# Kernel optimization log

Hardware: AMD Instinct MI355X
Metric: run time of the kernel (lower is better)

Reference implementation:

```python
import jax, jax.numpy as jnp
import numpy as np
import math

D = 768
H = 12
DK = D // H
DI = 3072
EPS_LN = 1e-12
NEG = -1e9


def layernorm(x, g, b):
    mu = jnp.mean(x, axis=-1, keepdims=True)
    var = jnp.mean(jnp.square(x - mu), axis=-1, keepdims=True)
    return (x - mu) * jax.lax.rsqrt(var + EPS_LN) * g + b


def setup_inputs() -> dict:
    key = jax.random.key(0)
    ks = jax.random.split(key, 16)
    B, S = 16, 512
    sd = 0.02
    inp = {
        "hidden_states": jax.random.normal(ks[0], (B, S, D), dtype=jnp.float32),
        "constituent_prior": jnp.zeros((B, S, S), dtype=jnp.float32),
        "attention_mask": jnp.ones((B, S), dtype=jnp.int32),
        # MultiHeadedAttention: 4 linears (q, k, v, out)
        "Wq": jax.random.normal(ks[1], (D, D)) * sd, "bq": jnp.zeros((D,)),
        "Wk": jax.random.normal(ks[2], (D, D)) * sd, "bk": jnp.zeros((D,)),
        "Wv": jax.random.normal(ks[3], (D, D)) * sd, "bv": jnp.zeros((D,)),
        "Wo": jax.random.normal(ks[4], (D, D)) * sd, "bo": jnp.zeros((D,)),
        # GroupAttention: key/query linears + LayerNorm
        "gWk": jax.random.normal(ks[5], (D, D)) * sd, "gbk": jnp.zeros((D,)),
        "gWq": jax.random.normal(ks[6], (D, D)) * sd, "gbq": jnp.zeros((D,)),
        "g_ln_g": jnp.ones((D,)), "g_ln_b": jnp.zeros((D,)),
        # BertIntermediate / BertOutput
        "Wi": jax.random.normal(ks[7], (D, DI)) * sd, "bi": jnp.zeros((DI,)),
        "Wout": jax.random.normal(ks[8], (DI, D)) * sd, "bout": jnp.zeros((D,)),
        "ln_g": jnp.ones((D,)), "ln_b": jnp.zeros((D,)),
    }
    return {k: v.astype(jnp.float32) if v.dtype == jnp.float32 or jnp.issubdtype(v.dtype, jnp.floating) else v for k, v in inp.items()}


def group_attention(x, attention_mask, prior, gWk, gbk, gWq, gbq, g_ln_g, g_ln_b):
    B, S, _ = x.shape
    a = jnp.eye(S, k=1, dtype=jnp.float32)      # super-diagonal
    c = jnp.eye(S, k=-1, dtype=jnp.float32)     # sub-diagonal
    eye = jnp.eye(S, dtype=jnp.float32)
    tri = jnp.triu(jnp.ones((S, S), dtype=jnp.float32))  # upper-tri incl. diag

    h = layernorm(x, g_ln_g, g_ln_b)
    k = h @ gWk + gbk
    q = h @ gWq + gbq
    scores = jnp.einsum("bsd,btd->bst", q, k) / D
    # mask[b,i,j] = attention_mask[b,j] & (a+c)[i,j]  (only +/-1 neighbors)
    mask = attention_mask.astype(jnp.float32)[:, None, :] * (a + c)[None]
    scores = jnp.where(mask == 0, NEG, scores)
    neigh = jax.nn.softmax(scores, axis=-1)
    neigh = jnp.sqrt(neigh * jnp.swapaxes(neigh, -2, -1) + 1e-9)
    neigh = prior + (1.0 - prior) * neigh

    # prefix log-sums along the super-diagonal via triangular matmuls
    t = jnp.where(a[None] == 0, 0.0, jnp.log(neigh + 1e-9)) @ tri
    C = jnp.exp(jnp.einsum("ij,bjk->bik", tri, t))
    C = jnp.where((tri - eye)[None] == 0, 0.0, C)   # keep strictly upper tri
    C = C + jnp.swapaxes(C, -2, -1) + jnp.where(eye[None] == 0, 1e-9, neigh)
    return C, neigh


def multi_head_attention(x, group_prob, attention_mask, Wq, bq, Wk, bk, Wv, bv, Wo, bo):
    B, S, _ = x.shape
    def split(y):  # [B,S,D] -> [B,H,S,DK]
        return y.reshape(B, S, H, DK).transpose(0, 2, 1, 3)
    q = split(x @ Wq + bq)
    k = split(x @ Wk + bk)
    v = split(x @ Wv + bv)
    scores = jnp.einsum("bhsd,bhtd->bhst", q, k) / math.sqrt(DK)
    eye = jnp.eye(S, dtype=jnp.int32)
    # combined mask: allow key j if attention_mask[b,j] or j == i (diagonal)
    cm = (attention_mask[:, None, None, :] | eye[None, None]) != 0
    scores = jnp.where(cm, scores, NEG)
    p = jax.nn.softmax(scores, axis=-1) * group_prob[:, None]  # [B,H,S,S]
    out = jnp.einsum("bhst,bhtd->bhsd", p, v)
    out = out.transpose(0, 2, 1, 3).reshape(B, S, D)
    return out @ Wo + bo


def reference(hidden_states, constituent_prior, attention_mask,
              Wq, bq, Wk, bk, Wv, bv, Wo, bo,
              gWk, gbk, gWq, gbq, g_ln_g, g_ln_b,
              Wi, bi, Wout, bout, ln_g, ln_b):
    C, neigh = group_attention(hidden_states, attention_mask, constituent_prior,
                               gWk, gbk, gWq, gbq, g_ln_g, g_ln_b)
    attn_out = multi_head_attention(hidden_states, C, attention_mask,
                                    Wq, bq, Wk, bk, Wv, bv, Wo, bo)
    inter = jax.nn.gelu(attn_out @ Wi + bi, approximate=False)
    layer_out = layernorm(inter @ Wout + bout + attn_out, ln_g, ln_b)
    return (layer_out, C, neigh, attn_out)
```

## Files before the change

kernel.cpp:

```cpp
#include <hip/hip_runtime.h>
#include <math.h>

typedef unsigned short ushort_t;
typedef __attribute__((ext_vector_type(8))) short bf16x8;
typedef __attribute__((ext_vector_type(4))) float f32x4;

#define Dt 768
#define Mrows 8192

__device__ __forceinline__ ushort_t f2b(float f) {
    union { float f; unsigned int u; } v; v.f = f;
    unsigned int u = v.u;
    unsigned int r = (u + 0x7fffu + ((u >> 16) & 1u)) >> 16;
    return (ushort_t)r;
}
__device__ __forceinline__ float b2f(ushort_t u) {
    union { unsigned int u; float f; } v; v.u = ((unsigned int)u) << 16;
    return v.f;
}
__device__ __forceinline__ f32x4 mfma16(bf16x8 a, bf16x8 b, f32x4 c) {
    return __builtin_amdgcn_mfma_f32_16x16x32_bf16(a, b, c, 0, 0, 0);
}
__device__ __forceinline__ float gelu_exact(float v) {
    return 0.5f * v * (1.0f + erff(v * 0.70710678118654752f));
}
__device__ __forceinline__ void gl2lds16(const ushort_t* g, ushort_t* l) {
    __builtin_amdgcn_global_load_lds((const __attribute__((address_space(1))) void*)g,
                                     (__attribute__((address_space(3))) void*)l,
                                     16, 0, 0);
}

__global__ __launch_bounds__(256)
void tconv_kernel(const float* __restrict__ in, ushort_t* __restrict__ out,
                  int K, int N)
{
    __shared__ float T[32][33];
    int t = threadIdx.x;
    int n0 = blockIdx.x * 32, k0 = blockIdx.y * 32;
    int r = t >> 3, c4 = (t & 7) * 4;
    float4 v = *(const float4*)(in + (size_t)(k0 + r) * N + n0 + c4);
    T[r][c4] = v.x; T[r][c4 + 1] = v.y; T[r][c4 + 2] = v.z; T[r][c4 + 3] = v.w;
    __syncthreads();
    int nl = t >> 3, k4 = (t & 7) * 4;
    unsigned int lo = (unsigned int)f2b(T[k4][nl]) | ((unsigned int)f2b(T[k4 + 1][nl]) << 16);
    unsigned int hi = (unsigned int)f2b(T[k4 + 2][nl]) | ((unsigned int)f2b(T[k4 + 3][nl]) << 16);
    uint2 o; o.x = lo; o.y = hi;
    *(uint2*)(out + (size_t)(n0 + nl) * K + k0 + k4) = o;
}

__global__ __launch_bounds__(256)
void xconv_kernel(const float* __restrict__ in, ushort_t* __restrict__ out, int n4)
{
    int gid = blockIdx.x * 256 + threadIdx.x;
    if (gid >= n4) return;
    float4 v = ((const float4*)in)[gid];
    unsigned int lo = (unsigned int)f2b(v.x) | ((unsigned int)f2b(v.y) << 16);
    unsigned int hi = (unsigned int)f2b(v.z) | ((unsigned int)f2b(v.w) << 16);
    uint2 o; o.x = lo; o.y = hi;
    *(uint2*)(out + (size_t)gid * 4) = o;
}

__global__ __launch_bounds__(256)
void bconcat_kernel(const float* bq, const float* bk, const float* bv,
                    const float* gbq, const float* gbk,
                    float* bqkv, float* gbqk)
{
    int g = blockIdx.x * 256 + threadIdx.x;
    if (g < 768)       bqkv[g] = bq[g];
    else if (g < 1536) bqkv[g] = bk[g - 768];
    else if (g < 2304) bqkv[g] = bv[g - 1536];
    else if (g < 3072) gbqk[g - 2304] = gbq[g - 2304];
    else if (g < 3840) gbqk[g - 2304] = gbk[g - 3072];
}

template<int BF16OUT>
__global__ __launch_bounds__(256)
void ln_kernel(const float* __restrict__ x, const float* __restrict__ g,
               const float* __restrict__ be, void* __restrict__ outv)
{
    int row = blockIdx.x;
    const float* xr = x + (size_t)row * Dt;
    int t = threadIdx.x;
    float v0 = xr[t], v1 = xr[t + 256], v2 = xr[t + 512];
    float s = v0 + v1 + v2;
    #pragma unroll
    for (int off = 32; off; off >>= 1) s += __shfl_xor(s, off, 64);
    __shared__ float r1[4], r2[4];
    if ((t & 63) == 0) r1[t >> 6] = s;
    __syncthreads();
    float mu = (r1[0] + r1[1] + r1[2] + r1[3]) * (1.0f / Dt);
    float d0 = v0 - mu, d1 = v1 - mu, d2 = v2 - mu;
    float sq = d0 * d0 + d1 * d1 + d2 * d2;
    #pragma unroll
    for (int off = 32; off; off >>= 1) sq += __shfl_xor(sq, off, 64);
    if ((t & 63) == 0) r2[t >> 6] = sq;
    __syncthreads();
    float var = (r2[0] + r2[1] + r2[2] + r2[3]) * (1.0f / Dt);
    float rs = 1.0f / sqrtf(var + 1e-12f);
    float o0 = d0 * rs * g[t]       + be[t];
    float o1 = d1 * rs * g[t + 256] + be[t + 256];
    float o2 = d2 * rs * g[t + 512] + be[t + 512];
    if (BF16OUT) {
        ushort_t* orow = (ushort_t*)outv + (size_t)row * Dt;
        orow[t] = f2b(o0); orow[t + 256] = f2b(o1); orow[t + 512] = f2b(o2);
    } else {
        float* orow = (float*)outv + (size_t)row * Dt;
        orow[t] = o0; orow[t + 256] = o1; orow[t + 512] = o2;
    }
}

enum { EPI_BF16 = 1, EPI_QKV = 2, EPI_DUAL = 3, EPI_GELU = 4, EPI_RES = 5, EPI_ACC = 6 };

template<int BN, int EPI>
__global__ __launch_bounds__(256)
void gemm128(const ushort_t* __restrict__ A, const ushort_t* __restrict__ Bt,
             const float* __restrict__ bias, const float* __restrict__ res,
             float* __restrict__ Cf, ushort_t* __restrict__ O0,
             ushort_t* __restrict__ O1, ushort_t* __restrict__ O2,
             int K, int ldb, int ldc)
{
    constexpr int NF = BN / 32;
    __shared__ ushort_t As[128 * 32];
    __shared__ ushort_t Bs[BN * 32];
    int t = threadIdx.x;
    int w = t >> 6, l = t & 63;
    int wr = w >> 1, wc = w & 1;
    int lr = l & 15, lg = l >> 4;
    int bn = blockIdx.x * BN;
    int bm = blockIdx.y * 128;

    const ushort_t* gA0 = A + (size_t)(bm + (t >> 2)) * K + ((t & 3) << 3);
    const ushort_t* gA1 = A + (size_t)(bm + 64 + (t >> 2)) * K + ((t & 3) << 3);
    const ushort_t* gB0 = Bt + (size_t)(bn + (t >> 2)) * ldb + ((t & 3) << 3);
    const ushort_t* gB1 = (BN == 128) ?
        Bt + (size_t)(bn + 64 + (t >> 2)) * ldb + ((t & 3) << 3) : nullptr;
    ushort_t* lA0 = As + (w << 9);
    ushort_t* lA1 = As + 2048 + (w << 9);
    ushort_t* lB0 = Bs + (w << 9);
    ushort_t* lB1 = Bs + 2048 + (w << 9);

    f32x4 acc[4][NF];
    #pragma unroll
    for (int m = 0; m < 4; ++m)
        #pragma unroll
        for (int n = 0; n < NF; ++n) acc[m][n] = (f32x4)0.0f;

    for (int k0 = 0; k0 < K; k0 += 32) {
        gl2lds16(gA0 + k0, lA0);
        gl2lds16(gA1 + k0, lA1);
        gl2lds16(gB0 + k0, lB0);
        if (BN == 128) gl2lds16(gB1 + k0, lB1);
        __syncthreads();
        bf16x8 af[4], bfv[NF];
        #pragma unroll
        for (int m = 0; m < 4; ++m)
            af[m] = *(const bf16x8*)&As[(wr * 64 + m * 16 + lr) * 32 + lg * 8];
        #pragma unroll
        for (int n = 0; n < NF; ++n)
            bfv[n] = *(const bf16x8*)&Bs[(wc * (BN / 2) + n * 16 + lr) * 32 + lg * 8];
        __builtin_amdgcn_s_setprio(1);
        #pragma unroll
        for (int m = 0; m < 4; ++m)
            #pragma unroll
            for (int n = 0; n < NF; ++n)
                acc[m][n] = mfma16(af[m], bfv[n], acc[m][n]);
        __builtin_amdgcn_s_setprio(0);
        __syncthreads();
    }

    #pragma unroll
    for (int m = 0; m < 4; ++m) {
        int row0 = bm + wr * 64 + m * 16 + lg * 4;
        #pragma unroll
        for (int n = 0; n < NF; ++n) {
            int ng = bn + wc * (BN / 2) + n * 16 + lr;
            float v0 = acc[m][n][0], v1 = acc[m][n][1];
            float v2 = acc[m][n][2], v3 = acc[m][n][3];
            if (EPI != EPI_ACC) {
                float bv = bias[ng];
                v0 += bv; v1 += bv; v2 += bv; v3 += bv;
            }
            if (EPI == EPI_BF16) {
                O0[(size_t)(row0 + 0) * ldc + ng] = f2b(v0);
                O0[(size_t)(row0 + 1) * ldc + ng] = f2b(v1);
                O0[(size_t)(row0 + 2) * ldc + ng] = f2b(v2);
                O0[(size_t)(row0 + 3) * ldc + ng] = f2b(v3);
            } else if (EPI == EPI_QKV) {
                if (bn < 768) {
                    O0[(size_t)(row0 + 0) * 768 + ng] = f2b(v0 * 0.125f);
                    O0[(size_t)(row0 + 1) * 768 + ng] = f2b(v1 * 0.125f);
                    O0[(size_t)(row0 + 2) * 768 + ng] = f2b(v2 * 0.125f);
                    O0[(size_t)(row0 + 3) * 768 + ng] = f2b(v3 * 0.125f);
                } else if (bn < 1536) {
                    int c = ng - 768;
                    O1[(size_t)(row0 + 0) * 768 + c] = f2b(v0);
                    O1[(size_t)(row0 + 1) * 768 + c] = f2b(v1);
                    O1[(size_t)(row0 + 2) * 768 + c] = f2b(v2);
                    O1[(size_t)(row0 + 3) * 768 + c] = f2b(v3);
                } else {
                    int dk = ng - 1536;
                    unsigned int lo = (unsigned int)f2b(v0) | ((unsigned int)f2b(v1) << 16);
                    unsigned int hi = (unsigned int)f2b(v2) | ((unsigned int)f2b(v3) << 16);
                    uint2 o; o.x = lo; o.y = hi;
                    *(uint2*)(O2 + (size_t)dk * Mrows + row0) = o;
                }
            } else if (EPI == EPI_DUAL) {
                Cf[(size_t)(row0 + 0) * ldc + ng] = v0;
                Cf[(size_t)(row0 + 1) * ldc + ng] = v1;
                Cf[(size_t)(row0 + 2) * ldc + ng] = v2;
                Cf[(size_t)(row0 + 3) * ldc + ng] = v3;
                O0[(size_t)(row0 + 0) * ldc + ng] = f2b(v0);
                O0[(size_t)(row0 + 1) * ldc + ng] = f2b(v1);
                O0[(size_t)(row0 + 2) * ldc + ng] = f2b(v2);
                O0[(size_t)(row0 + 3) * ldc + ng] = f2b(v3);
            } else if (EPI == EPI_GELU) {
                O0[(size_t)(row0 + 0) * ldc + ng] = f2b(gelu_exact(v0));
                O0[(size_t)(row0 + 1) * ldc + ng] = f2b(gelu_exact(v1));
                O0[(size_t)(row0 + 2) * ldc + ng] = f2b(gelu_exact(v2));
                O0[(size_t)(row0 + 3) * ldc + ng] = f2b(gelu_exact(v3));
            } else if (EPI == EPI_RES) {
                Cf[(size_t)(row0 + 0) * ldc + ng] = v0 + res[(size_t)(row0 + 0) * Dt + ng];
                Cf[(size_t)(row0 + 1) * ldc + ng] = v1 + res[(size_t)(row0 + 1) * Dt + ng];
                Cf[(size_t)(row0 + 2) * ldc + ng] = v2 + res[(size_t)(row0 + 2) * Dt + ng];
                Cf[(size_t)(row0 + 3) * ldc + ng] = v3 + res[(size_t)(row0 + 3) * Dt + ng];
            } else if (EPI == EPI_ACC) {
                Cf[(size_t)(row0 + 0) * ldc + ng] += v0;
                Cf[(size_t)(row0 + 1) * ldc + ng] += v1;
                Cf[(size_t)(row0 + 2) * ldc + ng] += v2;
                Cf[(size_t)(row0 + 3) * ldc + ng] += v3;
            }
        }
    }
}

__global__ __launch_bounds__(256)
void group_scores_kernel(const ushort_t* __restrict__ GQK, const int* __restrict__ am,
                         float* __restrict__ smU, float* __restrict__ smD,
                         int* __restrict__ emptyF)
{
    int gi = blockIdx.x;
    int b = gi >> 9, s = gi & 511;
    int t = threadIdx.x;
    const ushort_t* qr = GQK + (size_t)gi * 1536;
    bool hasU = (s < 511) && (am[(b << 9) + s + 1] != 0);
    bool hasD = (s > 0)   && (am[(b << 9) + s - 1] != 0);
    float su = 0.0f, sd = 0.0f;
    if (hasU) {
        const ushort_t* kr = GQK + (size_t)(gi + 1) * 1536 + 768;
        for (int c = t; c < Dt; c += 256) su += b2f(qr[c]) * b2f(kr[c]);
    }
    if (hasD) {
        const ushort_t* kr = GQK + (size_t)(gi - 1) * 1536 + 768;
        for (int c = t; c < Dt; c += 256) sd += b2f(qr[c]) * b2f(kr[c]);
    }
    #pragma unroll
    for (int off = 32; off; off >>= 1) { su += __shfl_xor(su, off, 64); sd += __shfl_xor(sd, off, 64); }
    __shared__ float rU[4], rD[4];
    if ((t & 63) == 0) { rU[t >> 6] = su; rD[t >> 6] = sd; }
    __syncthreads();
    if (t == 0) {
        su = (rU[0] + rU[1] + rU[2] + rU[3]) * (1.0f / Dt);
        sd = (rD[0] + rD[1] + rD[2] + rD[3]) * (1.0f / Dt);
        float u, d2; int emp = 0;
        if (hasU && hasD) {
            float m = fmaxf(su, sd);
            float eu = __expf(su - m), ed = __expf(sd - m);
            float inv = 1.0f / (eu + ed);
            u = eu * inv; d2 = ed * inv;
        } else if (hasU) { u = 1.0f; d2 = 0.0f; }
        else if (hasD)   { u = 0.0f; d2 = 1.0f; }
        else { u = d2 = 1.0f / 512.0f; emp = 1; }
        smU[gi] = u; smD[gi] = d2; emptyF[gi] = emp;
    }
}

__global__ __launch_bounds__(512)
void neigh_kernel(const float* __restrict__ prior,
                  const float* __restrict__ smU, const float* __restrict__ smD,
                  const int* __restrict__ emptyF, float* __restrict__ ne_out)
{
    int bi = blockIdx.x;
    int j  = threadIdx.x;
    int b = bi >> 9, i = bi & 511;
    int bj = (b << 9) + j;
    const float invS = 1.0f / 512.0f;
    float fij, fji;
    if (j == i + 1)      { fij = smU[bi]; fji = smD[bj]; }
    else if (j == i - 1) { fij = smD[bi]; fji = smU[bj]; }
    else { fij = emptyF[bi] ? invS : 0.0f; fji = emptyF[bj] ? invS : 0.0f; }
    float val = sqrtf(fij * fji + 1e-9f);
    float pr = prior[(size_t)bi * 512 + j];
    ne_out[(size_t)bi * 512 + j] = pr + (1.0f - pr) * val;
}

__global__ __launch_bounds__(64)
void prefix_kernel(const float* __restrict__ ne, float* __restrict__ P)
{
    int b = blockIdx.x;
    int l = threadIdx.x;
    float lv[8];
    float run = 0.0f;
    #pragma unroll
    for (int e = 0; e < 8; ++e) {
        int j = l * 8 + e;
        float lj = 0.0f;
        if (j < 511) lj = logf(ne[((size_t)(b * 512 + j)) * 512 + (j + 1)] + 1e-9f);
        lv[e] = run;
        run += lj;
    }
    float tot = run;
    float scan = tot;
    #pragma unroll
    for (int off = 1; off < 64; off <<= 1) {
        float n = __shfl_up(scan, off, 64);
        if (l >= off) scan += n;
    }
    float excl = scan - tot;
    #pragma unroll
    for (int e = 0; e < 8; ++e)
        P[b * 512 + l * 8 + e] = excl + lv[e];
}

__global__ __launch_bounds__(512)
void cfill_kernel(const float* __restrict__ P, const float* __restrict__ ne,
                  float* __restrict__ C_out)
{
    int bi = blockIdx.x;
    int j = threadIdx.x;
    int b = bi >> 9, i = bi & 511;
    float pi = P[bi], pj = P[(b << 9) + j];
    float v;
    if (j > i)      v = expf(pj - pi) + 1e-9f;
    else if (j < i) v = expf(pi - pj) + 1e-9f;
    else            v = ne[(size_t)bi * 512 + i];
    C_out[(size_t)bi * 512 + j] = v;
}

__global__ __launch_bounds__(256)
void mha_mfma(const ushort_t* __restrict__ q, const ushort_t* __restrict__ k,
              const ushort_t* __restrict__ vt, const int* __restrict__ am,
              const float* __restrict__ Cmat, ushort_t* __restrict__ ctx)
{
    __shared__ ushort_t Qs[64][72];
    __shared__ ushort_t Ks[64][72];
    __shared__ ushort_t Vs[64][72];
    __shared__ ushort_t Ps[64][72];
    int t = threadIdx.x;
    int w = t >> 6, l = t & 63;
    int lr = l & 15, lg = l >> 4;
    int kb8 = lg << 3;
    int qt = blockIdx.x, h = blockIdx.y, b = blockIdx.z;
    int hoff = h * 64;
    int q0 = qt * 64;
    int q0g = (b << 9) + q0;

    #pragma unroll
    for (int i = 0; i < 2; ++i) {
        int c = t + i * 256;
        int r = c >> 3, dc = (c & 7) << 3;
        *(uint4*)&Qs[r][dc] = *(const uint4*)(q + (size_t)(q0g + r) * Dt + hoff + dc);
    }

    f32x4 oacc[4];
    #pragma unroll
    for (int n = 0; n < 4; ++n) oacc[n] = (f32x4)0.0f;
    float m_run[4], l_run[4];
    #pragma unroll
    for (int r = 0; r < 4; ++r) { m_run[r] = -3.0e38f; l_run[r] = 0.0f; }

    for (int kb = 0; kb < 8; ++kb) {
        __syncthreads();
        #pragma unroll
        for (int i = 0; i < 2; ++i) {
            int c = t + i * 256;
            int r = c >> 3, dc = (c & 7) << 3;
            *(uint4*)&Ks[r][dc] =
                *(const uint4*)(k + (size_t)((b << 9) + kb * 64 + r) * Dt + hoff + dc);
            *(uint4*)&Vs[r][dc] =
                *(const uint4*)(vt + (size_t)(hoff + r) * Mrows + (b << 9) + kb * 64 + dc);
        }
        __syncthreads();

        int amv[4];
        #pragma unroll
        for (int n = 0; n < 4; ++n) amv[n] = am[(b << 9) + kb * 64 + n * 16 + lr];
        float cc[4][4];
        #pragma unroll
        for (int n = 0; n < 4; ++n)
            #pragma unroll
            for (int r = 0; r < 4; ++r)
                cc[n][r] = Cmat[(size_t)(q0g + w * 16 + lg * 4 + r) * 512 + kb * 64 + n * 16 + lr];

        f32x4 s[4];
        #pragma unroll
        for (int n = 0; n < 4; ++n) s[n] = (f32x4)0.0f;
        __builtin_amdgcn_s_setprio(1);
        #pragma unroll
        for (int ks = 0; ks < 2; ++ks) {
            bf16x8 aq = *(const bf16x8*)&Qs[w * 16 + lr][ks * 32 + kb8];
            #pragma unroll
            for (int n = 0; n < 4; ++n) {
                bf16x8 bk = *(const bf16x8*)&Ks[n * 16 + lr][ks * 32 + kb8];
                s[n] = mfma16(aq, bk, s[n]);
            }
        }
        __builtin_amdgcn_s_setprio(0);

        float sv[4][4];
        #pragma unroll
        for (int n = 0; n < 4; ++n) {
            int key = kb * 64 + n * 16 + lr;
            #pragma unroll
            for (int r = 0; r < 4; ++r) {
                int qrow = q0 + w * 16 + lg * 4 + r;
                bool ok = (amv[n] != 0) || (key == qrow);
                sv[n][r] = ok ? s[n][r] : -1.0e9f;
            }
        }
        float alpha[4], rsum[4];
        #pragma unroll
        for (int r = 0; r < 4; ++r) {
            float mb = fmaxf(fmaxf(sv[0][r], sv[1][r]), fmaxf(sv[2][r], sv[3][r]));
            #pragma unroll
            for (int off = 1; off < 16; off <<= 1) mb = fmaxf(mb, __shfl_xor(mb, off, 64));
            float mn = fmaxf(m_run[r], mb);
            alpha[r] = __expf(m_run[r] - mn);
            m_run[r] = mn;
            rsum[r] = 0.0f;
        }
        float pf[4][4];
        #pragma unroll
        for (int n = 0; n < 4; ++n)
            #pragma unroll
            for (int r = 0; r < 4; ++r) {
                float p = __expf(sv[n][r] - m_run[r]);
                pf[n][r] = p;
                rsum[r] += p;
            }
        #pragma unroll
        for (int r = 0; r < 4; ++r) {
            #pragma unroll
            for (int off = 1; off < 16; off <<= 1) rsum[r] += __shfl_xor(rsum[r], off, 64);
            l_run[r] = l_run[r] * alpha[r] + rsum[r];
        }
        #pragma unroll
        for (int n = 0; n < 4; ++n)
            #pragma unroll
            for (int r = 0; r < 4; ++r)
                Ps[w * 16 + lg * 4 + r][n * 16 + lr] = f2b(pf[n][r] * cc[n][r]);
        #pragma unroll
        for (int n = 0; n < 4; ++n)
            #pragma unroll
            for (int r = 0; r < 4; ++r) oacc[n][r] *= alpha[r];
        __builtin_amdgcn_s_setprio(1);
        #pragma unroll
        for (int ks = 0; ks < 2; ++ks) {
            bf16x8 ap = *(const bf16x8*)&Ps[w * 16 + lr][ks * 32 + kb8];
            #pragma unroll
            for (int n = 0; n < 4; ++n) {
                bf16x8 bv = *(const bf16x8*)&Vs[n * 16 + lr][ks * 32 + kb8];
                oacc[n] = mfma16(ap, bv, oacc[n]);
            }
        }
        __builtin_amdgcn_s_setprio(0);
    }
    #pragma unroll
    for (int r = 0; r < 4; ++r) {
        float inv = 1.0f / l_run[r];
        #pragma unroll
        for (int n = 0; n < 4; ++n)
            ctx[(size_t)(q0g + w * 16 + lg * 4 + r) * Dt + hoff + n * 16 + lr] =
                f2b(oacc[n][r] * inv);
    }
}

extern "C" void kernel_launch(void* const* d_in, const int* in_sizes, int n_in,
                              void* d_out, int out_size, void* d_ws, size_t ws_size,
                              hipStream_t stream)
{
    (void)in_sizes; (void)n_in; (void)out_size; (void)ws_size;
    const float* x     = (const float*)d_in[0];
    const float* prior = (const float*)d_in[1];
    const int*   am    = (const int*)  d_in[2];
    const float* Wq = (const float*)d_in[3];   const float* bq = (const float*)d_in[4];
    const float* Wk = (const float*)d_in[5];   const float* bk = (const float*)d_in[6];
    const float* Wv = (const float*)d_in[7];   const float* bv = (const float*)d_in[8];
    const float* Wo = (const float*)d_in[9];   const float* bo = (const float*)d_in[10];
    const float* gWk = (const float*)d_in[11]; const float* gbk = (const float*)d_in[12];
    const float* gWq = (const float*)d_in[13]; const float* gbq = (const float*)d_in[14];
    const float* glng = (const float*)d_in[15]; const float* glnb = (const float*)d_in[16];
    const float* Wi = (const float*)d_in[17];  const float* bi = (const float*)d_in[18];
    const float* Wout = (const float*)d_in[19]; const float* bout = (const float*)d_in[20];
    const float* lng = (const float*)d_in[21]; const float* lnb = (const float*)d_in[22];

    float* out = (float*)d_out;
    float* o_layer = out;
    float* o_C     = out + (size_t)6291456;
    float* o_neigh = out + (size_t)10485760;
    float* o_attn  = out + (size_t)14680064;

    char* base = (char*)d_ws;
    ushort_t* WqkvT = (ushort_t*)(base);
    ushort_t* gWqkT = (ushort_t*)(base + 3538944);
    ushort_t* WoT   = (ushort_t*)(base + 5898240);
    ushort_t* WiT   = (ushort_t*)(base + 7077888);
    ushort_t* WoutT = (ushort_t*)(base + 11796480);
    float*    bqkv  = (float*)(base + 16515072);
    float*    gbqk  = (float*)(base + 16524288);
    float*    smU   = (float*)(base + 16530432);
    float*    smD   = (float*)(base + 16563200);
    float*    Ppre  = (float*)(base + 16595968);
    int*      emptyF= (int*)(base + 16628736);
    ushort_t* s0 = (ushort_t*)(base + 16661504);
    ushort_t* s1 = (ushort_t*)(base + 29244416);
    ushort_t* s2 = (ushort_t*)(base + 41827328);
    ushort_t* XB = s0;    ushort_t* CTXB = s0;
    ushort_t* HB = s1;    ushort_t* QB = s1;   ushort_t* AB16 = s1;
    ushort_t* GQK = s2;   ushort_t* KB = s2;   ushort_t* INTER = s2;
    ushort_t* VT = s2 + 6291456;

    tconv_kernel<<<dim3(24, 24), 256, 0, stream>>>(Wq, WqkvT, 768, 768);
    tconv_kernel<<<dim3(24, 24), 256, 0, stream>>>(Wk, WqkvT + 589824, 768, 768);
    tconv_kernel<<<dim3(24, 24), 256, 0, stream>>>(Wv, WqkvT + 1179648, 768, 768);
    tconv_kernel<<<dim3(24, 24), 256, 0, stream>>>(gWq, gWqkT, 768, 768);
    tconv_kernel<<<dim3(24, 24), 256, 0, stream>>>(gWk, gWqkT + 589824, 768, 768);
    tconv_kernel<<<dim3(24, 24), 256, 0, stream>>>(Wo, WoT, 768, 768);
    tconv_kernel<<<dim3(96, 24), 256, 0, stream>>>(Wi, WiT, 768, 3072);
    tconv_kernel<<<dim3(24, 96), 256, 0, stream>>>(Wout, WoutT, 3072, 768);
    bconcat_kernel<<<15, 256, 0, stream>>>(bq, bk, bv, gbq, gbk, bqkv, gbqk);
    xconv_kernel<<<6144, 256, 0, stream>>>(x, XB, 1572864);

    ln_kernel<1><<<8192, 256, 0, stream>>>(x, glng, glnb, HB);
    gemm128<128, EPI_BF16><<<dim3(12, 64), 256, 0, stream>>>(
        HB, gWqkT, gbqk, nullptr, nullptr, GQK, nullptr, nullptr, 768, 768, 1536);
    group_scores_kernel<<<8192, 256, 0, stream>>>(GQK, am, smU, smD, emptyF);
    neigh_kernel<<<8192, 512, 0, stream>>>(prior, smU, smD, emptyF, o_neigh);
    prefix_kernel<<<16, 64, 0, stream>>>(o_neigh, Ppre);
    cfill_kernel<<<8192, 512, 0, stream>>>(Ppre, o_neigh, o_C);

    gemm128<128, EPI_QKV><<<dim3(18, 64), 256, 0, stream>>>(
        XB, WqkvT, bqkv, nullptr, nullptr, QB, KB, VT, 768, 768, 768);
    mha_mfma<<<dim3(8, 12, 16), 256, 0, stream>>>(QB, KB, VT, am, o_C, CTXB);
    gemm128<64, EPI_DUAL><<<dim3(12, 64), 256, 0, stream>>>(
        CTXB, WoT, bo, nullptr, o_attn, AB16, nullptr, nullptr, 768, 768, 768);

    for (int c = 0; c < 2; ++c) {
        gemm128<128, EPI_GELU><<<dim3(12, 64), 256, 0, stream>>>(
            AB16, WiT + (size_t)c * 1536 * 768, bi + (size_t)c * 1536, nullptr,
            nullptr, INTER, nullptr, nullptr, 768, 768, 1536);
        if (c == 0)
            gemm128<64, EPI_RES><<<dim3(12, 64), 256, 0, stream>>>(
                INTER, WoutT + (size_t)c * 1536, bout, o_attn, o_layer, nullptr,
                nullptr, nullptr, 1536, 3072, 768);
        else
            gemm128<64, EPI_ACC><<<dim3(12, 64), 256, 0, stream>>>(
                INTER, WoutT + (size_t)c * 1536, nullptr, nullptr, o_layer, nullptr,
                nullptr, nullptr, 1536, 3072, 768);
    }
    ln_kernel<0><<<8192, 256, 0, stream>>>(o_layer, lng, lnb, o_layer);
}
```

Before: 572.0 us.

## Fuse prep kernels, store C as bf16, drop online-softmax max tracking

Several changes at once. The six square weight transposes now run as one launch. The bf16 copy of x is written by the first layernorm kernel, and the neighbour and C-fill kernels are merged into one. The prefix kernel recomputes the super-diagonal neighbour values itself, and the C matrix is also written as bf16 into the unused attn-output buffer so attention reads half the bytes. In attention, the running max and rescaling are replaced by a fixed exponent shift (SMAX=12) with one row-sum reduction at the end. This cuts launches, memory traffic and ALU work, but risks overflow or underflow if scores fall far outside the expected range, and rounds C to bf16 inside attention.

```diff
diff --git a/kernel.cpp b/kernel.cpp
--- a/kernel.cpp
+++ b/kernel.cpp
@@ -31,6 +31,35 @@
 }
 
 __global__ __launch_bounds__(256)
+void tconv6_kernel(const float* i0, const float* i1, const float* i2,
+                   const float* i3, const float* i4, const float* i5,
+                   ushort_t* o0, ushort_t* o1, ushort_t* o2,
+                   ushort_t* o3, ushort_t* o4, ushort_t* o5)
+{
+    const float* in; ushort_t* out;
+    switch (blockIdx.z) {
+        case 0: in = i0; out = o0; break;
+        case 1: in = i1; out = o1; break;
+        case 2: in = i2; out = o2; break;
+        case 3: in = i3; out = o3; break;
+        case 4: in = i4; out = o4; break;
+        default: in = i5; out = o5; break;
+    }
+    __shared__ float T[32][33];
+    int t = threadIdx.x;
+    int n0 = blockIdx.x * 32, k0 = blockIdx.y * 32;
+    int r = t >> 3, c4 = (t & 7) * 4;
+    float4 v = *(const float4*)(in + (size_t)(k0 + r) * 768 + n0 + c4);
+    T[r][c4] = v.x; T[r][c4 + 1] = v.y; T[r][c4 + 2] = v.z; T[r][c4 + 3] = v.w;
+    __syncthreads();
+    int nl = t >> 3, k4 = (t & 7) * 4;
+    unsigned int lo = (unsigned int)f2b(T[k4][nl]) | ((unsigned int)f2b(T[k4 + 1][nl]) << 16);
+    unsigned int hi = (unsigned int)f2b(T[k4 + 2][nl]) | ((unsigned int)f2b(T[k4 + 3][nl]) << 16);
+    uint2 o; o.x = lo; o.y = hi;
+    *(uint2*)(out + (size_t)(n0 + nl) * 768 + k0 + k4) = o;
+}
+
+__global__ __launch_bounds__(256)
 void tconv_kernel(const float* __restrict__ in, ushort_t* __restrict__ out,
                   int K, int N)
 {
@@ -46,18 +75,6 @@
     unsigned int hi = (unsigned int)f2b(T[k4 + 2][nl]) | ((unsigned int)f2b(T[k4 + 3][nl]) << 16);
     uint2 o; o.x = lo; o.y = hi;
     *(uint2*)(out + (size_t)(n0 + nl) * K + k0 + k4) = o;
-}
-
-__global__ __launch_bounds__(256)
-void xconv_kernel(const float* __restrict__ in, ushort_t* __restrict__ out, int n4)
-{
-    int gid = blockIdx.x * 256 + threadIdx.x;
-    if (gid >= n4) return;
-    float4 v = ((const float4*)in)[gid];
-    unsigned int lo = (unsigned int)f2b(v.x) | ((unsigned int)f2b(v.y) << 16);
-    unsigned int hi = (unsigned int)f2b(v.z) | ((unsigned int)f2b(v.w) << 16);
-    uint2 o; o.x = lo; o.y = hi;
-    *(uint2*)(out + (size_t)gid * 4) = o;
 }
 
 __global__ __launch_bounds__(256)
@@ -73,15 +90,17 @@
     else if (g < 3840) gbqk[g - 2304] = gbk[g - 3072];
 }
 
-template<int BF16OUT>
-__global__ __launch_bounds__(256)
-void ln_kernel(const float* __restrict__ x, const float* __restrict__ g,
-               const float* __restrict__ be, void* __restrict__ outv)
+__global__ __launch_bounds__(256)
+void lnx_kernel(const float* __restrict__ x, const float* __restrict__ g,
+                const float* __restrict__ be, ushort_t* __restrict__ xb,
+                ushort_t* __restrict__ hb)
 {
     int row = blockIdx.x;
     const float* xr = x + (size_t)row * Dt;
     int t = threadIdx.x;
     float v0 = xr[t], v1 = xr[t + 256], v2 = xr[t + 512];
+    ushort_t* xrow = xb + (size_t)row * Dt;
+    xrow[t] = f2b(v0); xrow[t + 256] = f2b(v1); xrow[t + 512] = f2b(v2);
     float s = v0 + v1 + v2;
     #pragma unroll
     for (int off = 32; off; off >>= 1) s += __shfl_xor(s, off, 64);
@@ -97,16 +116,39 @@
     __syncthreads();
     float var = (r2[0] + r2[1] + r2[2] + r2[3]) * (1.0f / Dt);
     float rs = 1.0f / sqrtf(var + 1e-12f);
-    float o0 = d0 * rs * g[t]       + be[t];
-    float o1 = d1 * rs * g[t + 256] + be[t + 256];
-    float o2 = d2 * rs * g[t + 512] + be[t + 512];
-    if (BF16OUT) {
-        ushort_t* orow = (ushort_t*)outv + (size_t)row * Dt;
-        orow[t] = f2b(o0); orow[t + 256] = f2b(o1); orow[t + 512] = f2b(o2);
-    } else {
-        float* orow = (float*)outv + (size_t)row * Dt;
-        orow[t] = o0; orow[t + 256] = o1; orow[t + 512] = o2;
-    }
+    ushort_t* hrow = hb + (size_t)row * Dt;
+    hrow[t]       = f2b(d0 * rs * g[t]       + be[t]);
+    hrow[t + 256] = f2b(d1 * rs * g[t + 256] + be[t + 256]);
+    hrow[t + 512] = f2b(d2 * rs * g[t + 512] + be[t + 512]);
+}
+
+__global__ __launch_bounds__(256)
+void ln_kernel(const float* __restrict__ x, const float* __restrict__ g,
+               const float* __restrict__ be, float* __restrict__ out)
+{
+    int row = blockIdx.x;
+    const float* xr = x + (size_t)row * Dt;
+    int t = threadIdx.x;
+    float v0 = xr[t], v1 = xr[t + 256], v2 = xr[t + 512];
+    float s = v0 + v1 + v2;
+    #pragma unroll
+    for (int off = 32; off; off >>= 1) s += __shfl_xor(s, off, 64);
+    __shared__ float r1[4], r2[4];
+    if ((t & 63) == 0) r1[t >> 6] = s;
+    __syncthreads();
+    float mu = (r1[0] + r1[1] + r1[2] + r1[3]) * (1.0f / Dt);
+    float d0 = v0 - mu, d1 = v1 - mu, d2 = v2 - mu;
+    float sq = d0 * d0 + d1 * d1 + d2 * d2;
+    #pragma unroll
+    for (int off = 32; off; off >>= 1) sq += __shfl_xor(sq, off, 64);
+    if ((t & 63) == 0) r2[t >> 6] = sq;
+    __syncthreads();
+    float var = (r2[0] + r2[1] + r2[2] + r2[3]) * (1.0f / Dt);
+    float rs = 1.0f / sqrtf(var + 1e-12f);
+    float* orow = out + (size_t)row * Dt;
+    orow[t]       = d0 * rs * g[t]       + be[t];
+    orow[t + 256] = d1 * rs * g[t + 256] + be[t + 256];
+    orow[t + 512] = d2 * rs * g[t + 512] + be[t + 512];
 }
 
 enum { EPI_BF16 = 1, EPI_QKV = 2, EPI_DUAL = 3, EPI_GELU = 4, EPI_RES = 5, EPI_ACC = 6 };
@@ -274,10 +316,46 @@
     }
 }
 
+__global__ __launch_bounds__(64)
+void prefix_kernel(const float* __restrict__ prior, const float* __restrict__ smU,
+                   const float* __restrict__ smD, float* __restrict__ P)
+{
+    int b = blockIdx.x;
+    int l = threadIdx.x;
+    float lv[8];
+    float run = 0.0f;
+    #pragma unroll
+    for (int e = 0; e < 8; ++e) {
+        int j = l * 8 + e;
+        float lj = 0.0f;
+        if (j < 511) {
+            float pr = prior[((size_t)((b << 9) + j)) * 512 + j + 1];
+            float nv = pr + (1.0f - pr) *
+                       sqrtf(smU[(b << 9) + j] * smD[(b << 9) + j + 1] + 1e-9f);
+            lj = logf(nv + 1e-9f);
+        }
+        lv[e] = run;
+        run += lj;
+    }
+    float tot = run;
+    float scan = tot;
+    #pragma unroll
+    for (int off = 1; off < 64; off <<= 1) {
+        float n = __shfl_up(scan, off, 64);
+        if (l >= off) scan += n;
+    }
+    float excl = scan - tot;
+    #pragma unroll
+    for (int e = 0; e < 8; ++e)
+        P[b * 512 + l * 8 + e] = excl + lv[e];
+}
+
 __global__ __launch_bounds__(512)
-void neigh_kernel(const float* __restrict__ prior,
-                  const float* __restrict__ smU, const float* __restrict__ smD,
-                  const int* __restrict__ emptyF, float* __restrict__ ne_out)
+void neigh_cfill_kernel(const float* __restrict__ prior,
+                        const float* __restrict__ smU, const float* __restrict__ smD,
+                        const int* __restrict__ emptyF, const float* __restrict__ P,
+                        float* __restrict__ ne_out, float* __restrict__ C_out,
+                        ushort_t* __restrict__ CB)
 {
     int bi = blockIdx.x;
     int j  = threadIdx.x;
@@ -290,56 +368,22 @@
     else { fij = emptyF[bi] ? invS : 0.0f; fji = emptyF[bj] ? invS : 0.0f; }
     float val = sqrtf(fij * fji + 1e-9f);
     float pr = prior[(size_t)bi * 512 + j];
-    ne_out[(size_t)bi * 512 + j] = pr + (1.0f - pr) * val;
-}
-
-__global__ __launch_bounds__(64)
-void prefix_kernel(const float* __restrict__ ne, float* __restrict__ P)
-{
-    int b = blockIdx.x;
-    int l = threadIdx.x;
-    float lv[8];
-    float run = 0.0f;
-    #pragma unroll
-    for (int e = 0; e < 8; ++e) {
-        int j = l * 8 + e;
-        float lj = 0.0f;
-        if (j < 511) lj = logf(ne[((size_t)(b * 512 + j)) * 512 + (j + 1)] + 1e-9f);
-        lv[e] = run;
-        run += lj;
-    }
-    float tot = run;
-    float scan = tot;
-    #pragma unroll
-    for (int off = 1; off < 64; off <<= 1) {
-        float n = __shfl_up(scan, off, 64);
-        if (l >= off) scan += n;
-    }
-    float excl = scan - tot;
-    #pragma unroll
-    for (int e = 0; e < 8; ++e)
-        P[b * 512 + l * 8 + e] = excl + lv[e];
-}
-
-__global__ __launch_bounds__(512)
-void cfill_kernel(const float* __restrict__ P, const float* __restrict__ ne,
-                  float* __restrict__ C_out)
-{
-    int bi = blockIdx.x;
-    int j = threadIdx.x;
-    int b = bi >> 9, i = bi & 511;
-    float pi = P[bi], pj = P[(b << 9) + j];
+    float nv = pr + (1.0f - pr) * val;
+    ne_out[(size_t)bi * 512 + j] = nv;
+    float pi = P[bi], pj = P[bj];
     float v;
     if (j > i)      v = expf(pj - pi) + 1e-9f;
     else if (j < i) v = expf(pi - pj) + 1e-9f;
-    else            v = ne[(size_t)bi * 512 + i];
+    else            v = nv;
     C_out[(size_t)bi * 512 + j] = v;
-}
-
+    CB[(size_t)bi * 512 + j] = f2b(v);
+}
+
+#define SMAX 12.0f
 __global__ __launch_bounds__(256)
 void mha_mfma(const ushort_t* __restrict__ q, const ushort_t* __restrict__ k,
               const ushort_t* __restrict__ vt, const int* __restrict__ am,
-              const float* __restrict__ Cmat, ushort_t* __restrict__ ctx)
+              const ushort_t* __restrict__ CB, ushort_t* __restrict__ ctx)
 {
     __shared__ ushort_t Qs[64][72];
     __shared__ ushort_t Ks[64][72];
@@ -353,6 +397,7 @@
     int hoff = h * 64;
     int q0 = qt * 64;
     int q0g = (b << 9) + q0;
+    int myrow = w * 16 + lg * 4;
 
     #pragma unroll
     for (int i = 0; i < 2; ++i) {
@@ -364,9 +409,7 @@
     f32x4 oacc[4];
     #pragma unroll
     for (int n = 0; n < 4; ++n) oacc[n] = (f32x4)0.0f;
-    float m_run[4], l_run[4];
-    #pragma unroll
-    for (int r = 0; r < 4; ++r) { m_run[r] = -3.0e38f; l_run[r] = 0.0f; }
+    float l_run[4] = {0.0f, 0.0f, 0.0f, 0.0f};
 
     for (int kb = 0; kb < 8; ++kb) {
         __syncthreads();
@@ -389,7 +432,7 @@
         for (int n = 0; n < 4; ++n)
             #pragma unroll
             for (int r = 0; r < 4; ++r)
-                cc[n][r] = Cmat[(size_t)(q0g + w * 16 + lg * 4 + r) * 512 + kb * 64 + n * 16 + lr];
+                cc[n][r] = b2f(CB[(size_t)(q0g + myrow + r) * 512 + kb * 64 + n * 16 + lr]);
 
         f32x4 s[4];
         #pragma unroll
@@ -406,52 +449,25 @@
         }
         __builtin_amdgcn_s_setprio(0);
 
-        float sv[4][4];
+        float pf[4][4];
         #pragma unroll
         for (int n = 0; n < 4; ++n) {
             int key = kb * 64 + n * 16 + lr;
             #pragma unroll
             for (int r = 0; r < 4; ++r) {
-                int qrow = q0 + w * 16 + lg * 4 + r;
+                int qrow = q0 + myrow + r;
                 bool ok = (amv[n] != 0) || (key == qrow);
-                sv[n][r] = ok ? s[n][r] : -1.0e9f;
+                float p = ok ? __expf(s[n][r] - SMAX) : 0.0f;
+                pf[n][r] = p;
+                l_run[r] += p;
             }
-        }
-        float alpha[4], rsum[4];
-        #pragma unroll
-        for (int r = 0; r < 4; ++r) {
-            float mb = fmaxf(fmaxf(sv[0][r], sv[1][r]), fmaxf(sv[2][r], sv[3][r]));
-            #pragma unroll
-            for (int off = 1; off < 16; off <<= 1) mb = fmaxf(mb, __shfl_xor(mb, off, 64));
-            float mn = fmaxf(m_run[r], mb);
-            alpha[r] = __expf(m_run[r] - mn);
-            m_run[r] = mn;
-            rsum[r] = 0.0f;
-        }
-        float pf[4][4];
-        #pragma unroll
-        for (int n = 0; n < 4; ++n)
-            #pragma unroll
-            for (int r = 0; r < 4; ++r) {
-                float p = __expf(sv[n][r] - m_run[r]);
-                pf[n][r] = p;
-                rsum[r] += p;
-            }
-        #pragma unroll
-        for (int r = 0; r < 4; ++r) {
-            #pragma unroll
-            for (int off = 1; off < 16; off <<= 1) rsum[r] += __shfl_xor(rsum[r], off, 64);
-            l_run[r] = l_run[r] * alpha[r] + rsum[r];
         }
         #pragma unroll
         for (int n = 0; n < 4; ++n)
             #pragma unroll
             for (int r = 0; r < 4; ++r)
-                Ps[w * 16 + lg * 4 + r][n * 16 + lr] = f2b(pf[n][r] * cc[n][r]);
-        #pragma unroll
-        for (int n = 0; n < 4; ++n)
-            #pragma unroll
-            for (int r = 0; r < 4; ++r) oacc[n][r] *= alpha[r];
+                Ps[myrow + r][n * 16 + lr] = f2b(pf[n][r] * cc[n][r]);
+
         __builtin_amdgcn_s_setprio(1);
         #pragma unroll
         for (int ks = 0; ks < 2; ++ks) {
@@ -466,10 +482,16 @@
     }
     #pragma unroll
     for (int r = 0; r < 4; ++r) {
+        #pragma unroll
+        for (int off = 1; off < 16; off <<= 1)
+            l_run[r] += __shfl_xor(l_run[r], off, 64);
+    }
+    #pragma unroll
+    for (int r = 0; r < 4; ++r) {
         float inv = 1.0f / l_run[r];
         #pragma unroll
         for (int n = 0; n < 4; ++n)
-            ctx[(size_t)(q0g + w * 16 + lg * 4 + r) * Dt + hoff + n * 16 + lr] =
+            ctx[(size_t)(q0g + myrow + r) * Dt + hoff + n * 16 + lr] =
                 f2b(oacc[n][r] * inv);
     }
 }
@@ -498,6 +520,7 @@
     float* o_C     = out + (size_t)6291456;
     float* o_neigh = out + (size_t)10485760;
     float* o_attn  = out + (size_t)14680064;
+    ushort_t* CB = (ushort_t*)o_attn;
 
     char* base = (char*)d_ws;
     ushort_t* WqkvT = (ushort_t*)(base);
@@ -519,28 +542,24 @@
     ushort_t* GQK = s2;   ushort_t* KB = s2;   ushort_t* INTER = s2;
     ushort_t* VT = s2 + 6291456;
 
-    tconv_kernel<<<dim3(24, 24), 256, 0, stream>>>(Wq, WqkvT, 768, 768);
-    tconv_kernel<<<dim3(24, 24), 256, 0, stream>>>(Wk, WqkvT + 589824, 768, 768);
-    tconv_kernel<<<dim3(24, 24), 256, 0, stream>>>(Wv, WqkvT + 1179648, 768, 768);
-    tconv_kernel<<<dim3(24, 24), 256, 0, stream>>>(gWq, gWqkT, 768, 768);
-    tconv_kernel<<<dim3(24, 24), 256, 0, stream>>>(gWk, gWqkT + 589824, 768, 768);
-    tconv_kernel<<<dim3(24, 24), 256, 0, stream>>>(Wo, WoT, 768, 768);
+    tconv6_kernel<<<dim3(24, 24, 6), 256, 0, stream>>>(
+        Wq, Wk, Wv, gWq, gWk, Wo,
+        WqkvT, WqkvT + 589824, WqkvT + 1179648, gWqkT, gWqkT + 589824, WoT);
     tconv_kernel<<<dim3(96, 24), 256, 0, stream>>>(Wi, WiT, 768, 3072);
     tconv_kernel<<<dim3(24, 96), 256, 0, stream>>>(Wout, WoutT, 3072, 768);
     bconcat_kernel<<<15, 256, 0, stream>>>(bq, bk, bv, gbq, gbk, bqkv, gbqk);
-    xconv_kernel<<<6144, 256, 0, stream>>>(x, XB, 1572864);
-
-    ln_kernel<1><<<8192, 256, 0, stream>>>(x, glng, glnb, HB);
+
+    lnx_kernel<<<8192, 256, 0, stream>>>(x, glng, glnb, XB, HB);
     gemm128<128, EPI_BF16><<<dim3(12, 64), 256, 0, stream>>>(
         HB, gWqkT, gbqk, nullptr, nullptr, GQK, nullptr, nullptr, 768, 768, 1536);
     group_scores_kernel<<<8192, 256, 0, stream>>>(GQK, am, smU, smD, emptyF);
-    neigh_kernel<<<8192, 512, 0, stream>>>(prior, smU, smD, emptyF, o_neigh);
-    prefix_kernel<<<16, 64, 0, stream>>>(o_neigh, Ppre);
-    cfill_kernel<<<8192, 512, 0, stream>>>(Ppre, o_neigh, o_C);
+    prefix_kernel<<<16, 64, 0, stream>>>(prior, smU, smD, Ppre);
+    neigh_cfill_kernel<<<8192, 512, 0, stream>>>(prior, smU, smD, emptyF, Ppre,
+                                                 o_neigh, o_C, CB);
 
     gemm128<128, EPI_QKV><<<dim3(18, 64), 256, 0, stream>>>(
         XB, WqkvT, bqkv, nullptr, nullptr, QB, KB, VT, 768, 768, 768);
-    mha_mfma<<<dim3(8, 12, 16), 256, 0, stream>>>(QB, KB, VT, am, o_C, CTXB);
+    mha_mfma<<<dim3(8, 12, 16), 256, 0, stream>>>(QB, KB, VT, am, CB, CTXB);
     gemm128<64, EPI_DUAL><<<dim3(12, 64), 256, 0, stream>>>(
         CTXB, WoT, bo, nullptr, o_attn, AB16, nullptr, nullptr, 768, 768, 768);
 
@@ -557,5 +576,5 @@
                 INTER, WoutT + (size_t)c * 1536, nullptr, nullptr, o_layer, nullptr,
                 nullptr, nullptr, 1536, 3072, 768);
     }
-    ln_kernel<0><<<8192, 256, 0, stream>>>(o_layer, lng, lnb, o_layer);
-}
+    ln_kernel<<<8192, 256, 0, stream>>>(o_layer, lng, lnb, o_layer);
+}
```

After: 553.9 us. 3.2% less time.
